# Performance work log

Hardware: AMD Instinct MI355X
Metric: run time of the kernel (lower is better)

Reference implementation:

```python
import jax, jax.numpy as jnp
import numpy as np

N, NFEAT, NHID1, NHID2, NCLASS = 16384, 512, 256, 128, 8


def setup_inputs() -> dict:
    key = jax.random.key(0)
    ks = jax.random.split(key, 8)
    x = jax.random.normal(ks[0], (N, NFEAT), dtype=jnp.float32)
    adj = jax.random.uniform(ks[1], (N, N), dtype=jnp.float32)
    W1 = jax.random.normal(ks[2], (NFEAT, NHID1), dtype=jnp.float32) * (1.0 / np.sqrt(NFEAT))
    b1 = jnp.zeros((NHID1,), dtype=jnp.float32)
    W2 = jax.random.normal(ks[3], (NHID1, NHID2), dtype=jnp.float32) * (1.0 / np.sqrt(NHID1))
    b2 = jnp.zeros((NHID2,), dtype=jnp.float32)
    W3 = jax.random.normal(ks[4], (NHID2, NCLASS), dtype=jnp.float32) * (1.0 / np.sqrt(NHID2))
    b3 = jnp.zeros((NCLASS,), dtype=jnp.float32)
    return {"x": x, "adj": adj, "W1": W1, "b1": b1, "W2": W2, "b2": b2, "W3": W3, "b3": b3}


def _gc(x, adj, W, b):
    # GraphConvolution (Kipf): support = x @ W; out = adj @ support + b
    return adj @ (x @ W) + b


def reference(x, adj, W1, b1, W2, b2, W3, b3):
    # eval mode: dropout is identity
    h = jax.nn.relu(_gc(x, adj, W1, b1))
    h = jax.nn.relu(_gc(h, adj, W2, b2))
    h = _gc(h, adj, W3, b3)
    return jax.nn.log_softmax(h, axis=1)
```

## Files before the change

kernel.cpp:

```cpp
#include <hip/hip_runtime.h>
#include <hip/hip_bf16.h>

#define NROW 16384
#define NFEATC 512
#define NH1 256
#define NH2 128
#define NCLS 8

typedef __attribute__((ext_vector_type(8))) short short8;
typedef __attribute__((ext_vector_type(4))) float f32x4;

__device__ __forceinline__ ushort f2bf(float f) {
  union { float f; unsigned u; } v; v.f = f;
  unsigned r = v.u + 0x7FFFu + ((v.u >> 16) & 1u);
  return (ushort)(r >> 16);
}
__device__ __forceinline__ float bf2f(ushort h) {
  union { unsigned u; float f; } v; v.u = ((unsigned)h) << 16; return v.f;
}

__global__ __launch_bounds__(256) void transpose_conv(
    const float* __restrict__ in, ushort* __restrict__ out, int K, int N) {
  int idx = blockIdx.x * 256 + threadIdx.x;
  if (idx < K * N) {
    int k = idx / N, n = idx % N;
    out[(size_t)n * K + k] = f2bf(in[idx]);
  }
}

template<int BM, int BN, int WM, int WN, int KSPLIT, bool AFP32, int OUTM, bool KREV, int MINW>
__global__ __launch_bounds__(256, MINW) void gemm_pipe(
    const void* __restrict__ Ap, const ushort* __restrict__ BT,
    void* __restrict__ Outp, ushort* __restrict__ adjBF,
    const int nm, const int nn, const int M, const int N, const int K)
{
  constexpr int BK = 64, LDSK = BK + 8;
  constexpr int MR = WM / 16, NR = WN / 16;
  constexpr int nWc = BN / WN;
  static_assert((BM / WM) * (BN / WN) == 4, "4 waves");
  constexpr int AELEM = BM * BK / 256, ATPR = BK / AELEM;
  constexpr int BELEM = BN * BK / 256, BTPR = BK / BELEM;
  constexpr int A4s = AFP32 ? AELEM / 4 : 1;
  constexpr int A8s = AFP32 ? 1 : AELEM / 8;
  constexpr int B8s = (BELEM >= 8) ? BELEM / 8 : 1;

  __shared__ ushort As[2][BM * LDSK];
  __shared__ ushort Bs[2][BN * LDSK];

  const int t = threadIdx.x, l = t & 63, wid = t >> 6;
  const int wr0 = (wid / nWc) * WM, wc0 = (wid % nWc) * WN;

  const int cpx = gridDim.x >> 3;
  const int flat = (blockIdx.x & 7) * cpx + (blockIdx.x >> 3);
  const int n_blk = flat % nn;
  const int m_blk = (flat / nn) % nm;
  const int ksl = flat / (nn * nm);
  const int bm0 = m_blk * BM, bn0 = n_blk * BN;
  const int kper = K / KSPLIT, kbase = ksl * kper;
  const int NT = kper / BK;

  const int ar = t / ATPR, ak = (t % ATPR) * AELEM;
  const int br = t / BTPR, bk = (t % BTPR) * BELEM;

  const float*  Af = (const float*)Ap + (size_t)(bm0 + ar) * K + kbase + ak;
  const ushort* Ab = (const ushort*)Ap + (size_t)(bm0 + ar) * K + kbase + ak;
  const ushort* Bp = BT + (size_t)(bn0 + br) * K + kbase + bk;
  ushort* adjW = adjBF ? (adjBF + (size_t)(bm0 + ar) * K + kbase + ak) : nullptr;
  const bool wbf = AFP32 && (adjW != nullptr) && (n_blk == 0);

  f32x4 acc[MR][NR] = {};

  auto loadRegs = [&](float4 (&aF)[A4s], short8 (&aB)[A8s],
                      short8 (&bV)[B8s], ushort4& b4, int it) {
    const int ko = (KREV ? (NT - 1 - it) : it) * BK;
    if constexpr (AFP32) {
      #pragma unroll
      for (int c = 0; c < A4s; c++) aF[c] = *(const float4*)(Af + ko + 4 * c);
    } else {
      #pragma unroll
      for (int c = 0; c < A8s; c++) aB[c] = *(const short8*)(Ab + ko + 8 * c);
    }
    if constexpr (BELEM >= 8) {
      #pragma unroll
      for (int c = 0; c < B8s; c++) bV[c] = *(const short8*)(Bp + ko + 8 * c);
    } else {
      b4 = *(const ushort4*)(Bp + ko);
    }
  };

  auto writeLds = [&](int buf, float4 (&aF)[A4s], short8 (&aB)[A8s],
                      short8 (&bV)[B8s], ushort4& b4, int it) {
    const int ko = (KREV ? (NT - 1 - it) : it) * BK;
    if constexpr (AFP32) {
      #pragma unroll
      for (int c = 0; c < A4s; c++) {
        ushort4 v;
        v.x = f2bf(aF[c].x); v.y = f2bf(aF[c].y);
        v.z = f2bf(aF[c].z); v.w = f2bf(aF[c].w);
        *(ushort4*)&As[buf][ar * LDSK + ak + 4 * c] = v;
        if (wbf) *(ushort4*)(adjW + ko + 4 * c) = v;
      }
    } else {
      #pragma unroll
      for (int c = 0; c < A8s; c++)
        *(short8*)&As[buf][ar * LDSK + ak + 8 * c] = aB[c];
    }
    if constexpr (BELEM >= 8) {
      #pragma unroll
      for (int c = 0; c < B8s; c++)
        *(short8*)&Bs[buf][br * LDSK + bk + 8 * c] = bV[c];
    } else {
      *(ushort4*)&Bs[buf][br * LDSK + bk] = b4;
    }
  };

  auto compute = [&](int buf) {
    const int rr = l & 15;
    #pragma unroll
    for (int kk = 0; kk < 2; kk++) {
      const int kb = kk * 32 + (l >> 4) * 8;
      short8 af[MR], bfv[NR];
      #pragma unroll
      for (int m = 0; m < MR; m++)
        af[m] = *(short8*)&As[buf][(wr0 + m * 16 + rr) * LDSK + kb];
      #pragma unroll
      for (int n = 0; n < NR; n++)
        bfv[n] = *(short8*)&Bs[buf][(wc0 + n * 16 + rr) * LDSK + kb];
      #pragma unroll
      for (int m = 0; m < MR; m++)
        #pragma unroll
        for (int n = 0; n < NR; n++)
          acc[m][n] = __builtin_amdgcn_mfma_f32_16x16x32_bf16(af[m], bfv[n], acc[m][n], 0, 0, 0);
    }
  };

  float4 XaF[A4s], YaF[A4s];
  short8 XaB[A8s], YaB[A8s];
  short8 XbV[B8s], YbV[B8s];
  ushort4 Xb4, Yb4;

  loadRegs(XaF, XaB, XbV, Xb4, 0);
  writeLds(0, XaF, XaB, XbV, Xb4, 0);
  loadRegs(XaF, XaB, XbV, Xb4, 1);
  __syncthreads();

  for (int it = 0; it < NT; it += 2) {
    if (it + 2 < NT) loadRegs(YaF, YaB, YbV, Yb4, it + 2);
    compute(0);
    if (it + 1 < NT) writeLds(1, XaF, XaB, XbV, Xb4, it + 1);
    __syncthreads();
    if (it + 3 < NT) loadRegs(XaF, XaB, XbV, Xb4, it + 3);
    if (it + 1 < NT) compute(1);
    if (it + 2 < NT) writeLds(0, YaF, YaB, YbV, Yb4, it + 2);
    __syncthreads();
  }

  #pragma unroll
  for (int m = 0; m < MR; m++) {
    const int row = bm0 + wr0 + m * 16 + (l >> 4) * 4;
    #pragma unroll
    for (int n = 0; n < NR; n++) {
      const int col = bn0 + wc0 + n * 16 + (l & 15);
      if constexpr (OUTM == 1) {
        ushort4 v;
        v.x = f2bf(acc[m][n][0]); v.y = f2bf(acc[m][n][1]);
        v.z = f2bf(acc[m][n][2]); v.w = f2bf(acc[m][n][3]);
        *(ushort4*)((ushort*)Outp + (size_t)col * M + row) = v;
      } else {
        float* o = (float*)Outp + (size_t)ksl * M * N;
        #pragma unroll
        for (int r = 0; r < 4; r++)
          o[(size_t)(row + r) * N + col] = acc[m][n][r];
      }
    }
  }
}

__global__ __launch_bounds__(256) void reduce_relu(
    const float* __restrict__ part, const float* __restrict__ bias,
    ushort* __restrict__ out, const int MN, const int N, const int KS) {
  const int i4 = (blockIdx.x * 256 + threadIdx.x) * 4;
  if (i4 >= MN) return;
  float4 s = *(const float4*)(part + i4);
  for (int k = 1; k < KS; k++) {
    float4 p = *(const float4*)(part + (size_t)k * MN + i4);
    s.x += p.x; s.y += p.y; s.z += p.z; s.w += p.w;
  }
  const int col = i4 % N;
  float4 b = *(const float4*)(bias + col);
  ushort4 v;
  v.x = f2bf(fmaxf(s.x + b.x, 0.0f));
  v.y = f2bf(fmaxf(s.y + b.y, 0.0f));
  v.z = f2bf(fmaxf(s.z + b.z, 0.0f));
  v.w = f2bf(fmaxf(s.w + b.w, 0.0f));
  *(ushort4*)(out + i4) = v;
}

__global__ __launch_bounds__(256) void mm_small(
    const ushort* __restrict__ h2, const float* __restrict__ W3,
    ushort* __restrict__ s3T) {
  __shared__ float w[NH2 * NCLS];
  for (int i = threadIdx.x; i < NH2 * NCLS; i += 256) w[i] = W3[i];
  __syncthreads();
  const int m = blockIdx.x * 256 + threadIdx.x;
  float acc[8] = {};
  const ushort* row = h2 + (size_t)m * NH2;
  #pragma unroll
  for (int c = 0; c < NH2 / 8; c++) {
    short8 v = *(const short8*)(row + c * 8);
    #pragma unroll
    for (int j = 0; j < 8; j++) {
      float h = bf2f((ushort)v[j]);
      const int k = c * 8 + j;
      #pragma unroll
      for (int n = 0; n < 8; n++) acc[n] += h * w[k * 8 + n];
    }
  }
  #pragma unroll
  for (int n = 0; n < 8; n++) s3T[(size_t)n * NROW + m] = f2bf(acc[n]);
  #pragma unroll
  for (int n = 8; n < 16; n++) s3T[(size_t)n * NROW + m] = 0;
}

__global__ __launch_bounds__(256) void final_reduce(
    const float* __restrict__ part, const float* __restrict__ b3,
    float* __restrict__ out) {
  const int m = blockIdx.x * 256 + threadIdx.x;
  float4 s0 = make_float4(0, 0, 0, 0), s1 = make_float4(0, 0, 0, 0);
  #pragma unroll
  for (int k = 0; k < 4; k++) {
    const float4* p = (const float4*)(part + ((size_t)k * NROW + m) * 16);
    float4 a = p[0], b = p[1];
    s0.x += a.x; s0.y += a.y; s0.z += a.z; s0.w += a.w;
    s1.x += b.x; s1.y += b.y; s1.z += b.z; s1.w += b.w;
  }
  float v[8];
  v[0] = s0.x + b3[0]; v[1] = s0.y + b3[1]; v[2] = s0.z + b3[2]; v[3] = s0.w + b3[3];
  v[4] = s1.x + b3[4]; v[5] = s1.y + b3[5]; v[6] = s1.z + b3[6]; v[7] = s1.w + b3[7];
  float mx = v[0];
  #pragma unroll
  for (int n = 1; n < 8; n++) mx = fmaxf(mx, v[n]);
  float s = 0.0f;
  #pragma unroll
  for (int n = 0; n < 8; n++) s += expf(v[n] - mx);
  const float lse = logf(s) + mx;
  float4* o = (float4*)(out + (size_t)m * 8);
  o[0] = make_float4(v[0] - lse, v[1] - lse, v[2] - lse, v[3] - lse);
  o[1] = make_float4(v[4] - lse, v[5] - lse, v[6] - lse, v[7] - lse);
}

extern "C" void kernel_launch(void* const* d_in, const int* in_sizes, int n_in,
                              void* d_out, int out_size, void* d_ws, size_t ws_size,
                              hipStream_t stream) {
  const float* x   = (const float*)d_in[0];
  const float* adj = (const float*)d_in[1];
  const float* W1  = (const float*)d_in[2];
  const float* b1  = (const float*)d_in[3];
  const float* W2  = (const float*)d_in[4];
  const float* b2  = (const float*)d_in[5];
  const float* W3  = (const float*)d_in[6];
  const float* b3  = (const float*)d_in[7];
  float* out = (float*)d_out;

  char* ws = (char*)d_ws;
  size_t off = 0;
  ushort* W1T = (ushort*)(ws + off); off += (size_t)NH1 * NFEATC * 2;
  ushort* W2T = (ushort*)(ws + off); off += (size_t)NH2 * NH1 * 2;
  ushort* s1T = (ushort*)(ws + off); off += (size_t)NH1 * NROW * 2;
  ushort* h1  = (ushort*)(ws + off); off += (size_t)NROW * NH1 * 2;
  ushort* s2T = (ushort*)(ws + off); off += (size_t)NH2 * NROW * 2;
  ushort* h2  = (ushort*)(ws + off); off += (size_t)NROW * NH2 * 2;
  ushort* s3T = (ushort*)(ws + off); off += (size_t)16 * NROW * 2;
  float*  part = (float*)(ws + off); off += (size_t)2 * NROW * NH1 * 4;
  ushort* adjBF = (ushort*)(ws + off); off += (size_t)NROW * NROW * 2;

  transpose_conv<<<(NFEATC * NH1 + 255) / 256, 256, 0, stream>>>(W1, W1T, NFEATC, NH1);
  transpose_conv<<<(NH1 * NH2 + 255) / 256, 256, 0, stream>>>(W2, W2T, NH1, NH2);

  gemm_pipe<64, 128, 32, 64, 1, true, 1, false, 2><<<512, 256, 0, stream>>>(
      x, W1T, s1T, nullptr, 256, 2, NROW, NH1, NFEATC);
  gemm_pipe<128, 128, 64, 64, 2, true, 2, false, 2><<<512, 256, 0, stream>>>(
      adj, s1T, part, adjBF, 128, 2, NROW, NH1, NROW);
  reduce_relu<<<(NROW * NH1 / 4 + 255) / 256, 256, 0, stream>>>(
      part, b1, h1, NROW * NH1, NH1, 2);
  gemm_pipe<64, 128, 32, 64, 1, false, 1, false, 2><<<256, 256, 0, stream>>>(
      h1, W2T, s2T, nullptr, 256, 1, NROW, NH2, NH1);
  gemm_pipe<128, 128, 64, 64, 4, false, 2, true, 2><<<512, 256, 0, stream>>>(
      adjBF, s2T, part, nullptr, 128, 1, NROW, NH2, NROW);
  reduce_relu<<<(NROW * NH2 / 4 + 255) / 256, 256, 0, stream>>>(
      part, b2, h2, NROW * NH2, NH2, 4);
  mm_small<<<NROW / 256, 256, 0, stream>>>(h2, W3, s3T);
  gemm_pipe<128, 16, 32, 16, 4, false, 2, false, 3><<<512, 256, 0, stream>>>(
      adjBF, s3T, part, nullptr, 128, 1, NROW, 16, NROW);
  final_reduce<<<NROW / 256, 256, 0, stream>>>(part, b3, out);
}
```

Baseline: 867.6 us.

## Drop split-K for big adjacency GEMMs, fuse bias+ReLU epilogue, use smaller tiles

The two large adj@support GEMMs now use 64x64 tiles without split-K and apply bias and ReLU in the GEMM epilogue, writing bf16 directly. This removes the reduce_relu kernels and the fp32 partial-sum traffic. The pipeline becomes a simpler single-register-set double buffer, the K-reversal option is removed, tile sizes and grids change for every GEMM, and mm_small uses 64-thread blocks. Smaller tiles mean adj is reread more often per output column block (4 or 2 n-blocks instead of 2 or 1), which raises global traffic. The shallower prefetch may also expose more latency.

```diff
diff --git a/kernel.cpp b/kernel.cpp
--- a/kernel.cpp
+++ b/kernel.cpp
@@ -28,10 +28,11 @@
   }
 }
 
-template<int BM, int BN, int WM, int WN, int KSPLIT, bool AFP32, int OUTM, bool KREV, int MINW>
+template<int BM, int BN, int WM, int WN, int KSPLIT, bool AFP32, int OUTM, bool WADJ, int MINW>
 __global__ __launch_bounds__(256, MINW) void gemm_pipe(
     const void* __restrict__ Ap, const ushort* __restrict__ BT,
     void* __restrict__ Outp, ushort* __restrict__ adjBF,
+    const float* __restrict__ bias,
     const int nm, const int nn, const int M, const int N, const int K)
 {
   constexpr int BK = 64, LDSK = BK + 8;
@@ -65,14 +66,18 @@
   const float*  Af = (const float*)Ap + (size_t)(bm0 + ar) * K + kbase + ak;
   const ushort* Ab = (const ushort*)Ap + (size_t)(bm0 + ar) * K + kbase + ak;
   const ushort* Bp = BT + (size_t)(bn0 + br) * K + kbase + bk;
-  ushort* adjW = adjBF ? (adjBF + (size_t)(bm0 + ar) * K + kbase + ak) : nullptr;
-  const bool wbf = AFP32 && (adjW != nullptr) && (n_blk == 0);
+  ushort* adjW = WADJ ? (adjBF + (size_t)(bm0 + ar) * K + kbase + ak) : nullptr;
+  const bool wbf = WADJ && (n_blk == 0);
 
   f32x4 acc[MR][NR] = {};
 
-  auto loadRegs = [&](float4 (&aF)[A4s], short8 (&aB)[A8s],
-                      short8 (&bV)[B8s], ushort4& b4, int it) {
-    const int ko = (KREV ? (NT - 1 - it) : it) * BK;
+  float4 aF[A4s];
+  short8 aB[A8s];
+  short8 bV[B8s];
+  ushort4 b4;
+
+  auto loadRegs = [&](int it) {
+    const int ko = it * BK;
     if constexpr (AFP32) {
       #pragma unroll
       for (int c = 0; c < A4s; c++) aF[c] = *(const float4*)(Af + ko + 4 * c);
@@ -88,9 +93,8 @@
     }
   };
 
-  auto writeLds = [&](int buf, float4 (&aF)[A4s], short8 (&aB)[A8s],
-                      short8 (&bV)[B8s], ushort4& b4, int it) {
-    const int ko = (KREV ? (NT - 1 - it) : it) * BK;
+  auto writeLds = [&](int buf, int it) {
+    const int ko = it * BK;
     if constexpr (AFP32) {
       #pragma unroll
       for (int c = 0; c < A4s; c++) {
@@ -134,24 +138,14 @@
     }
   };
 
-  float4 XaF[A4s], YaF[A4s];
-  short8 XaB[A8s], YaB[A8s];
-  short8 XbV[B8s], YbV[B8s];
-  ushort4 Xb4, Yb4;
-
-  loadRegs(XaF, XaB, XbV, Xb4, 0);
-  writeLds(0, XaF, XaB, XbV, Xb4, 0);
-  loadRegs(XaF, XaB, XbV, Xb4, 1);
+  loadRegs(0);
+  writeLds(0, 0);
   __syncthreads();
-
-  for (int it = 0; it < NT; it += 2) {
-    if (it + 2 < NT) loadRegs(YaF, YaB, YbV, Yb4, it + 2);
-    compute(0);
-    if (it + 1 < NT) writeLds(1, XaF, XaB, XbV, Xb4, it + 1);
-    __syncthreads();
-    if (it + 3 < NT) loadRegs(XaF, XaB, XbV, Xb4, it + 3);
-    if (it + 1 < NT) compute(1);
-    if (it + 2 < NT) writeLds(0, YaF, YaB, YbV, Yb4, it + 2);
+  for (int it = 0; it < NT; it++) {
+    const int cur = it & 1;
+    if (it + 1 < NT) loadRegs(it + 1);
+    compute(cur);
+    if (it + 1 < NT) writeLds(cur ^ 1, it + 1);
     __syncthreads();
   }
 
@@ -166,43 +160,29 @@
         v.x = f2bf(acc[m][n][0]); v.y = f2bf(acc[m][n][1]);
         v.z = f2bf(acc[m][n][2]); v.w = f2bf(acc[m][n][3]);
         *(ushort4*)((ushort*)Outp + (size_t)col * M + row) = v;
-      } else {
+      } else if constexpr (OUTM == 2) {
         float* o = (float*)Outp + (size_t)ksl * M * N;
         #pragma unroll
         for (int r = 0; r < 4; r++)
           o[(size_t)(row + r) * N + col] = acc[m][n][r];
+      } else {
+        const float bv = bias[col];
+        ushort* o = (ushort*)Outp;
+        #pragma unroll
+        for (int r = 0; r < 4; r++)
+          o[(size_t)(row + r) * N + col] = f2bf(fmaxf(acc[m][n][r] + bv, 0.0f));
       }
     }
   }
 }
 
-__global__ __launch_bounds__(256) void reduce_relu(
-    const float* __restrict__ part, const float* __restrict__ bias,
-    ushort* __restrict__ out, const int MN, const int N, const int KS) {
-  const int i4 = (blockIdx.x * 256 + threadIdx.x) * 4;
-  if (i4 >= MN) return;
-  float4 s = *(const float4*)(part + i4);
-  for (int k = 1; k < KS; k++) {
-    float4 p = *(const float4*)(part + (size_t)k * MN + i4);
-    s.x += p.x; s.y += p.y; s.z += p.z; s.w += p.w;
-  }
-  const int col = i4 % N;
-  float4 b = *(const float4*)(bias + col);
-  ushort4 v;
-  v.x = f2bf(fmaxf(s.x + b.x, 0.0f));
-  v.y = f2bf(fmaxf(s.y + b.y, 0.0f));
-  v.z = f2bf(fmaxf(s.z + b.z, 0.0f));
-  v.w = f2bf(fmaxf(s.w + b.w, 0.0f));
-  *(ushort4*)(out + i4) = v;
-}
-
-__global__ __launch_bounds__(256) void mm_small(
+__global__ __launch_bounds__(64) void mm_small(
     const ushort* __restrict__ h2, const float* __restrict__ W3,
     ushort* __restrict__ s3T) {
   __shared__ float w[NH2 * NCLS];
-  for (int i = threadIdx.x; i < NH2 * NCLS; i += 256) w[i] = W3[i];
+  for (int i = threadIdx.x; i < NH2 * NCLS; i += 64) w[i] = W3[i];
   __syncthreads();
-  const int m = blockIdx.x * 256 + threadIdx.x;
+  const int m = blockIdx.x * 64 + threadIdx.x;
   float acc[8] = {};
   const ushort* row = h2 + (size_t)m * NH2;
   #pragma unroll
@@ -271,26 +251,22 @@
   ushort* s2T = (ushort*)(ws + off); off += (size_t)NH2 * NROW * 2;
   ushort* h2  = (ushort*)(ws + off); off += (size_t)NROW * NH2 * 2;
   ushort* s3T = (ushort*)(ws + off); off += (size_t)16 * NROW * 2;
-  float*  part = (float*)(ws + off); off += (size_t)2 * NROW * NH1 * 4;
+  float*  part = (float*)(ws + off); off += (size_t)4 * NROW * 16 * 4;
   ushort* adjBF = (ushort*)(ws + off); off += (size_t)NROW * NROW * 2;
 
   transpose_conv<<<(NFEATC * NH1 + 255) / 256, 256, 0, stream>>>(W1, W1T, NFEATC, NH1);
   transpose_conv<<<(NH1 * NH2 + 255) / 256, 256, 0, stream>>>(W2, W2T, NH1, NH2);
 
-  gemm_pipe<64, 128, 32, 64, 1, true, 1, false, 2><<<512, 256, 0, stream>>>(
-      x, W1T, s1T, nullptr, 256, 2, NROW, NH1, NFEATC);
-  gemm_pipe<128, 128, 64, 64, 2, true, 2, false, 2><<<512, 256, 0, stream>>>(
-      adj, s1T, part, adjBF, 128, 2, NROW, NH1, NROW);
-  reduce_relu<<<(NROW * NH1 / 4 + 255) / 256, 256, 0, stream>>>(
-      part, b1, h1, NROW * NH1, NH1, 2);
-  gemm_pipe<64, 128, 32, 64, 1, false, 1, false, 2><<<256, 256, 0, stream>>>(
-      h1, W2T, s2T, nullptr, 256, 1, NROW, NH2, NH1);
-  gemm_pipe<128, 128, 64, 64, 4, false, 2, true, 2><<<512, 256, 0, stream>>>(
-      adjBF, s2T, part, nullptr, 128, 1, NROW, NH2, NROW);
-  reduce_relu<<<(NROW * NH2 / 4 + 255) / 256, 256, 0, stream>>>(
-      part, b2, h2, NROW * NH2, NH2, 4);
-  mm_small<<<NROW / 256, 256, 0, stream>>>(h2, W3, s3T);
-  gemm_pipe<128, 16, 32, 16, 4, false, 2, false, 3><<<512, 256, 0, stream>>>(
-      adjBF, s3T, part, nullptr, 128, 1, NROW, 16, NROW);
+  gemm_pipe<64, 64, 32, 32, 1, true, 1, false, 4><<<1024, 256, 0, stream>>>(
+      x, W1T, s1T, nullptr, nullptr, 256, 4, NROW, NH1, NFEATC);
+  gemm_pipe<64, 64, 32, 32, 1, true, 3, true, 4><<<1024, 256, 0, stream>>>(
+      adj, s1T, h1, adjBF, b1, 256, 4, NROW, NH1, NROW);
+  gemm_pipe<64, 64, 32, 32, 1, false, 1, false, 4><<<512, 256, 0, stream>>>(
+      h1, W2T, s2T, nullptr, nullptr, 256, 2, NROW, NH2, NH1);
+  gemm_pipe<64, 64, 32, 32, 1, false, 3, false, 4><<<512, 256, 0, stream>>>(
+      adjBF, s2T, h2, nullptr, b2, 256, 2, NROW, NH2, NROW);
+  mm_small<<<NROW / 64, 64, 0, stream>>>(h2, W3, s3T);
+  gemm_pipe<64, 16, 16, 16, 4, false, 2, false, 4><<<1024, 256, 0, stream>>>(
+      adjBF, s3T, part, nullptr, nullptr, 256, 1, NROW, 16, NROW);
   final_reduce<<<NROW / 256, 256, 0, stream>>>(part, b3, out);
 }
```

After: 1.115 ms. 1.29x slower.
